# Performance work log

Measured on AMD Instinct MI355X. Metric: run time of the kernel, lower is better.

The kernel has to match this reference:

```python
import jax, jax.numpy as jnp
import numpy as np

N_HEADS = 8
N_POINTS = 4
EPS = 1e-5


def _conv1x1(x, w, b):
    # x: [B,C,H,W], w: [O,C]
    return jnp.einsum('bchw,oc->bohw', x, w) + b[None, :, None, None]


def _gn(x, g, b, groups=32):
    B, C, H, W = x.shape
    xr = x.reshape(B, groups, C // groups, H, W)
    m = xr.mean((2, 3, 4), keepdims=True)
    v = xr.var((2, 3, 4), keepdims=True)
    xn = ((xr - m) * jax.lax.rsqrt(v + EPS)).reshape(B, C, H, W)
    return xn * g[None, :, None, None] + b[None, :, None, None]


def _ln(x, g, b):
    m = x.mean(-1, keepdims=True)
    v = x.var(-1, keepdims=True)
    return (x - m) * jax.lax.rsqrt(v + EPS) * g + b


def _ln_spec(x, g2, b2, n):
    # modality-specific LayerNorm: separate params for v tokens [:n] and i tokens [n:]
    return jnp.concatenate([_ln(x[:, :n], g2[0], b2[0]), _ln(x[:, n:], g2[1], b2[1])], 1)


def _sine_pos(h, w, d):
    nf = d // 2
    scale = 2.0 * np.pi
    ye = jnp.arange(1, h + 1, dtype=jnp.float32) / h * scale
    xe = jnp.arange(1, w + 1, dtype=jnp.float32) / w * scale
    dim_t = 10000.0 ** (2.0 * (jnp.arange(nf) // 2).astype(jnp.float32) / nf)
    def enc(e):
        p = e[:, None] / dim_t
        return jnp.stack([jnp.sin(p[:, 0::2]), jnp.cos(p[:, 1::2])], -1).reshape(e.shape[0], nf)
    py = enc(ye)  # [h,nf]
    px = enc(xe)  # [w,nf]
    pos = jnp.concatenate([jnp.broadcast_to(py[:, None, :], (h, w, nf)),
                           jnp.broadcast_to(px[None, :, :], (h, w, nf))], -1)
    return pos.reshape(h * w, d)


def _bilinear(vl, loc):
    # vl: [B,h,w,Hd,Dh] value for one level, loc: [B,Lq,Hd,P,2] normalized (x,y)
    B, h, w, Hd, Dh = vl.shape
    Lq, P = loc.shape[1], loc.shape[3]
    x = loc[..., 0] * w - 0.5
    y = loc[..., 1] * h - 0.5
    x0 = jnp.floor(x)
    y0 = jnp.floor(y)
    wx = x - x0
    wy = y - y0
    x0i = x0.astype(jnp.int32)
    y0i = y0.astype(jnp.int32)
    v2 = vl.reshape(B, h * w, Hd, Dh).transpose(0, 2, 1, 3)  # [B,Hd,HW,Dh]
    def g(ix, iy):
        valid = ((ix >= 0) & (ix < w) & (iy >= 0) & (iy < h)).astype(vl.dtype)
        flat = jnp.clip(iy, 0, h - 1) * w + jnp.clip(ix, 0, w - 1)  # [B,Lq,Hd,P]
        idx = flat.transpose(0, 2, 1, 3).reshape(B, Hd, Lq * P)
        gv = jnp.take_along_axis(v2, idx[..., None], axis=2)  # [B,Hd,Lq*P,Dh]
        gv = gv.reshape(B, Hd, Lq, P, Dh).transpose(0, 2, 1, 3, 4)  # [B,Lq,Hd,P,Dh]
        return gv * valid[..., None]
    return (g(x0i, y0i) * ((1 - wx) * (1 - wy))[..., None]
            + g(x0i + 1, y0i) * (wx * (1 - wy))[..., None]
            + g(x0i, y0i + 1) * ((1 - wx) * wy)[..., None]
            + g(x0i + 1, y0i + 1) * (wx * wy)[..., None])


def _deform_attn(q, src, ref, shapes, ow, ob, aww, awb, vw, vb, opw, opb):
    B, Len, D = src.shape
    L = len(shapes)
    Hd, P = N_HEADS, N_POINTS
    Dh = D // Hd
    value = src @ vw + vb
    off = (q @ ow + ob).reshape(B, Len, Hd, L, P, 2)
    aw = jax.nn.softmax((q @ aww + awb).reshape(B, Len, Hd, L * P), -1).reshape(B, Len, Hd, L, P)
    norm = jnp.array([[s[1], s[0]] for s in shapes], jnp.float32)  # (w,h) per level
    loc = ref[None, :, None, None, None, :] + off / norm[None, None, None, :, None, :]
    out = jnp.zeros((B, Len, Hd, Dh), value.dtype)
    start = 0
    for l, (hh, ww) in enumerate(shapes):
        vl = value[:, start:start + hh * ww].reshape(B, hh, ww, Hd, Dh)
        samp = _bilinear(vl, loc[:, :, :, l])  # [B,Len,Hd,P,Dh]
        out = out + (samp * aw[:, :, :, l, :, None]).sum(3)
        start += hh * ww
    return out.reshape(B, Len, D) @ opw + opb


def _forward(input_v, input_i, av_w, av_b, av_g, av_be, ai_w, ai_b, ai_g, ai_be,
             level_embed, off_w, off_b, aw_w, aw_b, vp_w, vp_b, op_w, op_b,
             ln1_g, ln1_b, ffn1_w, ffn1_b, ffn2_w, ffn2_b, ln2_g, ln2_b,
             as_w, as_b, as_g, as_be):
    b, c, h, w = input_v.shape
    D = av_w.shape[0]
    hw = h * w
    fv = _gn(_conv1x1(input_v, av_w, av_b), av_g, av_be)
    fi = _gn(_conv1x1(input_i, ai_w, ai_b), ai_g, ai_be)
    sv = fv.reshape(b, D, hw).transpose(0, 2, 1)
    si = fi.reshape(b, D, hw).transpose(0, 2, 1)
    src = jnp.concatenate([sv, si], 1)  # [b, 2hw, D]
    pos = _sine_pos(h, w, D)
    posf = jnp.concatenate([pos + level_embed[0], pos + level_embed[1]], 0)
    gx = (jnp.arange(w, dtype=jnp.float32) + 0.5) / w
    gy = (jnp.arange(h, dtype=jnp.float32) + 0.5) / h
    X, Y = jnp.meshgrid(gx, gy)
    ref1 = jnp.stack([X, Y], -1).reshape(hw, 2)
    ref = jnp.concatenate([ref1, ref1], 0)  # [2hw, 2]
    shapes = [(h, w), (h, w)]
    for i in range(off_w.shape[0]):
        q = src + posf
        attn = _deform_attn(q, src, ref, shapes, off_w[i], off_b[i], aw_w[i], aw_b[i],
                            vp_w[i], vp_b[i], op_w[i], op_b[i])
        src = _ln_spec(src + attn, ln1_g[i], ln1_b[i], hw)
        ff = jax.nn.relu(src @ ffn1_w[i] + ffn1_b[i]) @ ffn2_w[i] + ffn2_b[i]
        src = _ln_spec(src + ff, ln2_g[i], ln2_b[i], hw)
    out = src[:, :hw] + src[:, hw:]  # chunk along tokens, sum modalities
    out = out.transpose(0, 2, 1).reshape(b, D, h, w)
    return _gn(_conv1x1(out, as_w, as_b), as_g, as_be)


def setup_inputs():
    key = jax.random.key(0)
    B, C, H, W = 16, 768, 20, 20
    D, NL, Hd, L, P, Dff = 512, 6, N_HEADS, 2, N_POINTS, 1024
    ks = iter(jax.random.split(key, 64))
    def rn(shape, scale=0.02):
        return jax.random.normal(next(ks), shape, jnp.float32) * scale
    return {
        'input_v': jax.random.normal(next(ks), (B, C, H, W), jnp.float32),
        'input_i': jax.random.normal(next(ks), (B, C, H, W), jnp.float32),
        'av_w': rn((D, C)), 'av_b': jnp.zeros((D,)), 'av_g': jnp.ones((D,)), 'av_be': jnp.zeros((D,)),
        'ai_w': rn((D, C)), 'ai_b': jnp.zeros((D,)), 'ai_g': jnp.ones((D,)), 'ai_be': jnp.zeros((D,)),
        'level_embed': rn((L, D)),
        'off_w': rn((NL, D, Hd * L * P * 2)), 'off_b': rn((NL, Hd * L * P * 2), 0.5),
        'aw_w': rn((NL, D, Hd * L * P)), 'aw_b': jnp.zeros((NL, Hd * L * P)),
        'vp_w': rn((NL, D, D)), 'vp_b': jnp.zeros((NL, D)),
        'op_w': rn((NL, D, D)), 'op_b': jnp.zeros((NL, D)),
        'ln1_g': jnp.ones((NL, 2, D)), 'ln1_b': jnp.zeros((NL, 2, D)),
        'ffn1_w': rn((NL, D, Dff)), 'ffn1_b': jnp.zeros((NL, Dff)),
        'ffn2_w': rn((NL, Dff, D)), 'ffn2_b': jnp.zeros((NL, D)),
        'ln2_g': jnp.ones((NL, 2, D)), 'ln2_b': jnp.zeros((NL, 2, D)),
        'as_w': rn((C, D)), 'as_b': jnp.zeros((C,)), 'as_g': jnp.ones((C,)), 'as_be': jnp.zeros((C,)),
    }


def reference(input_v, input_i, av_w, av_b, av_g, av_be, ai_w, ai_b, ai_g, ai_be,
              level_embed, off_w, off_b, aw_w, aw_b, vp_w, vp_b, op_w, op_b,
              ln1_g, ln1_b, ffn1_w, ffn1_b, ffn2_w, ffn2_b, ln2_g, ln2_b,
              as_w, as_b, as_g, as_be):
    return _forward(input_v, input_i, av_w, av_b, av_g, av_be, ai_w, ai_b, ai_g, ai_be,
                    level_embed, off_w, off_b, aw_w, aw_b, vp_w, vp_b, op_w, op_b,
                    ln1_g, ln1_b, ffn1_w, ffn1_b, ffn2_w, ffn2_b, ln2_g, ln2_b,
                    as_w, as_b, as_g, as_be)
```

## Files before the change

kernel.cpp:

```cpp
#include <hip/hip_runtime.h>
#include <hip/hip_bf16.h>
#include <cstddef>
#include <math.h>


constexpr int kB   = 16;
constexpr int kCin = 768;
constexpr int kHW  = 400;
constexpr int kWpx = 20;
constexpr int kHpx = 20;
constexpr int kD   = 512;
constexpr int kLen = 800;
constexpr int kDff = 1024;
constexpr int kNL  = 6;
constexpr float kEps = 1e-5f;

typedef __attribute__((ext_vector_type(8))) short s8v;
typedef __attribute__((ext_vector_type(4))) short s4v;
typedef __attribute__((ext_vector_type(4))) float f4v;

__device__ __forceinline__ int swzk(int row, int k) {
  return (k & ~31) | ((((k >> 3) + (row >> 1)) & 3) << 3) | (k & 7);
}

__device__ __forceinline__ unsigned short f2b(float f) {
  union { __hip_bfloat16 h; unsigned short u; } cv;
  cv.h = __float2bfloat16(f);
  return cv.u;
}

__device__ __forceinline__ float b2f(unsigned short u) {
  return __uint_as_float(((unsigned)u) << 16);
}

__device__ __forceinline__ void gll(const unsigned short* g, unsigned short* l) {
  __builtin_amdgcn_global_load_lds(
      (const __attribute__((address_space(1))) unsigned int*)g,
      (__attribute__((address_space(3))) unsigned int*)l, 16, 0, 0);
}

__device__ __forceinline__ void breduce2(float& s, float& s2, float* sh) {
#pragma unroll
  for (int o = 32; o > 0; o >>= 1) {
    s  += __shfl_down(s, o);
    s2 += __shfl_down(s2, o);
  }
  const int wid = threadIdx.x >> 6, lane = threadIdx.x & 63;
  if (lane == 0) { sh[wid] = s; sh[4 + wid] = s2; }
  __syncthreads();
  if (threadIdx.x == 0) {
    sh[0] = sh[0] + sh[1] + sh[2] + sh[3];
    sh[4] = sh[4] + sh[5] + sh[6] + sh[7];
  }
  __syncthreads();
  s = sh[0]; s2 = sh[4];
}

template<int EPI>
__global__ __launch_bounds__(256)
void mgemm(const unsigned short* __restrict__ Abf,
           const unsigned short* __restrict__ Bw,
           const float* __restrict__ bias,
           const unsigned short* __restrict__ resb,
           float* __restrict__ Cf, unsigned short* __restrict__ Cb2,
           const float* __restrict__ aux,
           unsigned short* __restrict__ Cb,
           int K, int ldc, int Nreal)
{
  __shared__ unsigned short As[3][4096];
  __shared__ unsigned short Bs[3][4096];
  const int tid = threadIdx.x;
  const int w = tid >> 6, l = tid & 63;

  const int gx = gridDim.x;
  const int nwg = gx * gridDim.y;
  const int bid = blockIdx.y * gx + blockIdx.x;
  const int q = nwg >> 3, r = nwg & 7;
  const int xcd = bid & 7, idx = bid >> 3;
  const int wgid = (xcd < r ? xcd * (q + 1) : r * (q + 1) + (xcd - r) * q) + idx;
  const int m0 = (wgid / gx) * 128;
  const int n0 = (wgid % gx) * 128;

  if (EPI == 6 && m0 >= 6400) { Bw = resb; bias = aux; }

  f4v acc[4][4] = {};

  const int srow = w * 32 + (l >> 2);
  const unsigned short* ga0 = Abf + (size_t)(m0 + srow) * K + (l & 3) * 8;
  const unsigned short* ga1 = ga0 + (size_t)16 * K;
  const unsigned short* gb0 = Bw + (size_t)(n0 + srow) * K + (l & 3) * 8;
  const unsigned short* gb1 = gb0 + (size_t)16 * K;
  const int lb0 = (w * 32) * 32;
  const int lb1 = (w * 32 + 16) * 32;

  int aoff[4], boff[4];
#pragma unroll
  for (int f = 0; f < 4; f++) {
    const int ra = (w >> 1) * 64 + f * 16 + (l & 15);
    aoff[f] = ra * 32 + ((((l >> 4) + (ra >> 1)) & 3) << 3);
    const int rb = (w & 1) * 64 + f * 16 + (l & 15);
    boff[f] = rb * 32 + ((((l >> 4) + (rb >> 1)) & 3) << 3);
  }

#define STAGEG(ko, bi) do { \
    gll(ga0 + (ko), &As[bi][lb0]); gll(ga1 + (ko), &As[bi][lb1]); \
    gll(gb0 + (ko), &Bs[bi][lb0]); gll(gb1 + (ko), &Bs[bi][lb1]); } while (0)

  const int NT = K >> 5;
  STAGEG(0, 0);
  STAGEG(32, 1);

  int cur = 0;
  int bpre = 2;
  int kpre = 64;
  for (int t = 0; t < NT; ++t) {
    if (t + 1 < NT) asm volatile("s_waitcnt vmcnt(4)" ::: "memory");
    else            asm volatile("s_waitcnt vmcnt(0)" ::: "memory");
    __builtin_amdgcn_s_barrier();
    __builtin_amdgcn_sched_barrier(0);
    if (t + 2 < NT) STAGEG(kpre, bpre);
    s8v af[4], bf4[4];
#pragma unroll
    for (int f = 0; f < 4; f++) {
      af[f]  = *(const s8v*)&As[cur][aoff[f]];
      bf4[f] = *(const s8v*)&Bs[cur][boff[f]];
    }
    __builtin_amdgcn_s_setprio(1);
#pragma unroll
    for (int i = 0; i < 4; i++)
#pragma unroll
      for (int j = 0; j < 4; j++)
        acc[i][j] = __builtin_amdgcn_mfma_f32_16x16x32_bf16(af[i], bf4[j], acc[i][j], 0, 0, 0);
    __builtin_amdgcn_s_setprio(0);
    kpre += 32;
    bpre = (bpre == 2) ? 0 : bpre + 1;
    cur  = (cur == 2) ? 0 : cur + 1;
  }
#undef STAGEG

  const int colb = n0 + (w & 1) * 64;
  const int rowb = m0 + (w >> 1) * 64 + (l >> 4) * 4;
#pragma unroll
  for (int i = 0; i < 4; i++) {
#pragma unroll
    for (int j = 0; j < 4; j++) {
      const int col = colb + j * 16 + (l & 15);
      float bv;
      if (EPI == 4) bv = (col < kD) ? bias[col] : 0.0f;
      else          bv = bias[col];
#pragma unroll
      for (int r2 = 0; r2 < 4; r2++) {
        const int row = rowb + i * 16 + r2;
        float v = acc[i][j][r2] + bv;
        if (EPI == 1) {
          Cb[(size_t)row * ldc + swzk(row, col)] = f2b(fmaxf(v, 0.0f));
        } else if (EPI == 2) {
          v += b2f(resb[(size_t)row * kD + swzk(row, col)]);
          Cb[(size_t)row * kD + col] = f2b(v);
        } else if (EPI == 3) {
          const int bb = row / kHW, p = row % kHW;
          Cb[((size_t)bb * Nreal + col) * kHW + p] = f2b(v);
        } else if (EPI == 4) {
          if (col < kD) {
            Cb[(size_t)row * kD + col] = f2b(v);
          } else {
            const int c = col - kD;
            if (c < 192)
              Cb2[(size_t)row * 192 + c] = f2b(v + aux[(size_t)(row % kLen) * 192 + c]);
          }
        } else if (EPI == 5) {
          if (row < kLen) {
            const int ll = col >> 8, c = col & 255;
            if (c < 192)
              Cf[(((size_t)ll * kLen) + row) * 192 + c] = v;
          }
        } else {
          Cb[(size_t)row * kD + col] = f2b(v);
        }
      }
    }
  }
}

__device__ __forceinline__ void cvt8t(const float* __restrict__ W,
                                      unsigned short* __restrict__ out,
                                      int K, int N, int g)
{
  const int n = g % N;
  const int k = (g / N) * 8;
  s8v p;
#pragma unroll
  for (int j = 0; j < 8; j++) p[j] = (short)f2b(W[(size_t)(k + j) * N + n]);
  const int base = n * K + (k & ~31) + ((((k >> 3) + (n >> 1)) & 3) << 3);
  *(s8v*)&out[base] = p;
}

__global__ __launch_bounds__(256)
void cvt_all_k(const float* __restrict__ vp_w, const float* __restrict__ op_w,
               const float* __restrict__ off_w, const float* __restrict__ aw_w,
               const float* __restrict__ f1w_a, const float* __restrict__ f2w_a,
               unsigned short* __restrict__ wall)
{
  const int lyr = blockIdx.x / 832;
  int g = (blockIdx.x % 832) * 256 + threadIdx.x;
  unsigned short* wl = wall + (size_t)lyr * 1703936;
  if (g < 32768) { cvt8t(vp_w + (size_t)lyr * kD * kD, wl, 512, 512, g); return; }
  g -= 32768;
  if (g < 16384) {
    const int n = g & 255;
    const int k = (g >> 8) * 8;
    const float* ow  = off_w + (size_t)lyr * kD * 128;
    const float* aww = aw_w  + (size_t)lyr * kD * 64;
    s8v p;
#pragma unroll
    for (int j = 0; j < 8; j++) {
      float v = 0.0f;
      if (n < 128)      v = ow[(size_t)(k + j) * 128 + n];
      else if (n < 192) v = aww[(size_t)(k + j) * 64 + (n - 128)];
      p[j] = (short)f2b(v);
    }
    const int row = 512 + n;
    const int base = row * 512 + (k & ~31) + ((((k >> 3) + (row >> 1)) & 3) << 3);
    *(s8v*)&wl[base] = p;
    return;
  }
  g -= 16384;
  if (g < 32768) { cvt8t(op_w + (size_t)lyr * kD * kD, wl + 393216, 512, 512, g); return; }
  g -= 32768;
  if (g < 65536) { cvt8t(f1w_a + (size_t)lyr * kD * kDff, wl + 655360, 512, 1024, g); return; }
  g -= 65536;
  cvt8t(f2w_a + (size_t)lyr * kDff * kD, wl + 1179648, 1024, 512, g);
}

__global__ __launch_bounds__(256)
void pre_k(const float* __restrict__ level_embed,
           const float* __restrict__ off_w, const float* __restrict__ aw_w,
           const float* __restrict__ off_b, const float* __restrict__ aw_b,
           unsigned short* __restrict__ posfb,
           unsigned short* __restrict__ woaw_all, float* __restrict__ biasall)
{
  int g = blockIdx.x * 256 + threadIdx.x;
  if (g < 57344) {
    const int d0 = (g & 63) * 8;
    const int t  = g >> 6;
    s8v o;
    if (t >= kLen) {
#pragma unroll
      for (int j = 0; j < 8; j++) o[j] = 0;
    } else {
      const int lvl = t / kHW;
      const int tt = t % kHW;
      const int yy = tt / kWpx, xx = tt % kWpx;
#pragma unroll
      for (int j = 0; j < 8; j++) {
        const int d = d0 + j;
        const int dd = d & 255;
        const float e = (d < 256) ? ((float)(yy + 1) * (6.283185307179586f / kHpx))
                                  : ((float)(xx + 1) * (6.283185307179586f / kWpx));
        const float dimt = powf(10000.0f, (float)(dd >> 1) / 128.0f);
        const float pp = e / dimt;
        const float val = (dd & 1) ? cosf(pp) : sinf(pp);
        o[j] = (short)f2b(val + level_embed[lvl * kD + d]);
      }
    }
    *(s8v*)&posfb[(size_t)t * kD + swzk(t, d0)] = o;
    return;
  }
  g -= 57344;
  if (g < 98304) {
    const int l = g >> 14;
    const int gg = g & 16383;
    const int n = gg & 255;
    const int k = (gg >> 8) * 8;
    const float* ow = off_w + (size_t)l * kD * 128;
    const float* aww = aw_w + (size_t)l * kD * 64;
    s8v p;
#pragma unroll
    for (int j = 0; j < 8; j++) {
      float v = 0.0f;
      if (n < 128)      v = ow[(size_t)(k + j) * 128 + n];
      else if (n < 192) v = aww[(size_t)(k + j) * 64 + (n - 128)];
      p[j] = (short)f2b(v);
    }
    const int row = l * 256 + n;
    const int base = row * 512 + (k & ~31) + ((((k >> 3) + (row >> 1)) & 3) << 3);
    *(s8v*)&woaw_all[base] = p;
    return;
  }
  g -= 98304;
  if (g < 1536) {
    const int l = g >> 8, c = g & 255;
    float v = 0.0f;
    if (c < 128)      v = off_b[l * 128 + c];
    else if (c < 192) v = aw_b[l * 64 + (c - 128)];
    biasall[l * 256 + c] = v;
  }
}

__global__ void tincvt_k(const float* __restrict__ inv, const float* __restrict__ ini,
                         const float* __restrict__ W0, const float* __restrict__ W1,
                         unsigned short* __restrict__ out, unsigned short* __restrict__ wcs)
{
  __shared__ float t[16][17];
  const int bid = blockIdx.x;
  if (bid < 38400) {
    const int z = bid / 1200;
    const int rem = bid % 1200;
    const int c0 = (rem % 48) * 16, p0 = (rem / 48) * 16;
    const int mod = z >> 4, b = z & 15;
    const float* in = (mod ? ini : inv) + (size_t)b * kCin * kHW;
    const int tx = threadIdx.x & 15, ty = threadIdx.x >> 4;
    t[ty][tx] = in[((size_t)(c0 + ty)) * kHW + p0 + tx];
    __syncthreads();
    const int row = z * kHW + p0 + ty;
    const int c = c0 + tx;
    out[(size_t)row * kCin + swzk(row, c)] = f2b(t[tx][ty]);
    return;
  }
  int gid = (bid - 38400) * 256 + threadIdx.x;
  const float* W = W0;
  unsigned short* o = wcs;
  if (gid >= 49152) { gid -= 49152; W = W1; o = wcs + 393216; }
  const int n = gid / 96;
  const int k = (gid % 96) * 8;
  s8v p;
#pragma unroll
  for (int j = 0; j < 8; j++) p[j] = (short)f2b(W[(size_t)n * kCin + k + j]);
  const int base = n * kCin + (k & ~31) + ((((k >> 3) + (n >> 1)) & 3) << 3);
  *(s8v*)&o[base] = p;
}

__global__ __launch_bounds__(256)
void gn_stats_tok_k(const unsigned short* __restrict__ x, float* __restrict__ stats)
{
  __shared__ float sh[8];
  const int mb = blockIdx.x >> 5;
  const int g = blockIdx.x & 31;
  const unsigned short* xb = x + (size_t)mb * kHW * kD + g * 16;
  float s = 0.f, s2 = 0.f;
  for (int i = threadIdx.x; i < 800; i += 256) {
    const int p = i >> 1, half = i & 1;
    const s8v u = *(const s8v*)&xb[(size_t)p * kD + half * 8];
#pragma unroll
    for (int j = 0; j < 8; j++) {
      const float v = b2f((unsigned short)u[j]);
      s += v; s2 += v * v;
    }
  }
  breduce2(s, s2, sh);
  if (threadIdx.x == 0) {
    const float mean = s / (kHW * 16.0f);
    const float var  = s2 / (kHW * 16.0f) - mean * mean;
    stats[blockIdx.x * 2]     = mean;
    stats[blockIdx.x * 2 + 1] = rsqrtf(var + kEps);
  }
}

__global__ void gn_norm_tok_k(const unsigned short* __restrict__ x,
                              unsigned short* __restrict__ srcb,
                              const float* __restrict__ stats,
                              const float* __restrict__ gv, const float* __restrict__ bev,
                              const float* __restrict__ gi, const float* __restrict__ bei)
{
  const int gid = blockIdx.x * 256 + threadIdx.x;
  const int d0 = (gid & 63) * 8;
  const int rl = gid >> 6;
  const int mb = rl / kHW;
  const int p  = rl - mb * kHW;
  const int mod = mb >> 4, b = mb & 15;
  const int g = d0 >> 4;
  const float mean = stats[(mb * 32 + g) * 2];
  const float rstd = stats[(mb * 32 + g) * 2 + 1];
  const float* gam = mod ? gi : gv;
  const float* bet = mod ? bei : bev;
  const s8v u = *(const s8v*)&x[(size_t)rl * kD + d0];
  const int row = b * kLen + mod * kHW + p;
  s8v o;
#pragma unroll
  for (int j = 0; j < 8; j++)
    o[j] = (short)f2b((b2f((unsigned short)u[j]) - mean) * rstd * gam[d0 + j] + bet[d0 + j]);
  *(s8v*)&srcb[(size_t)row * kD + swzk(row, d0)] = o;
}

__global__ __launch_bounds__(256)
void gn_stats_ch_k(const unsigned short* __restrict__ x, float* __restrict__ stats)
{
  __shared__ float sh[8];
  const int b = blockIdx.x >> 5;
  const int g = blockIdx.x & 31;
  const unsigned short* xb = x + (size_t)b * kCin * kHW + (size_t)g * 24 * kHW;
  float s = 0.f, s2 = 0.f;
  for (int i = threadIdx.x; i < 1200; i += 256) {
    const s8v u = *(const s8v*)&xb[(size_t)i * 8];
#pragma unroll
    for (int j = 0; j < 8; j++) {
      const float v = b2f((unsigned short)u[j]);
      s += v; s2 += v * v;
    }
  }
  breduce2(s, s2, sh);
  if (threadIdx.x == 0) {
    const float mean = s / (24.0f * kHW);
    const float var  = s2 / (24.0f * kHW) - mean * mean;
    stats[blockIdx.x * 2]     = mean;
    stats[blockIdx.x * 2 + 1] = rsqrtf(var + kEps);
  }
}

__global__ void gn_norm_ch_k(const unsigned short* __restrict__ x, float* __restrict__ out,
                             const float* __restrict__ stats,
                             const float* __restrict__ gam, const float* __restrict__ bet)
{
  const int gid = blockIdx.x * 256 + threadIdx.x;
  const int idx8 = gid * 8;
  const int rest = idx8 / kHW;
  const int c = rest % kCin;
  const int b = rest / kCin;
  const int g = c / 24;
  const float mean = stats[(b * 32 + g) * 2];
  const float rstd = stats[(b * 32 + g) * 2 + 1];
  const float gg = gam[c], bb = bet[c];
  const s8v u = *(const s8v*)&x[idx8];
  float4 o0, o1;
  o0.x = (b2f((unsigned short)u[0]) - mean) * rstd * gg + bb;
  o0.y = (b2f((unsigned short)u[1]) - mean) * rstd * gg + bb;
  o0.z = (b2f((unsigned short)u[2]) - mean) * rstd * gg + bb;
  o0.w = (b2f((unsigned short)u[3]) - mean) * rstd * gg + bb;
  o1.x = (b2f((unsigned short)u[4]) - mean) * rstd * gg + bb;
  o1.y = (b2f((unsigned short)u[5]) - mean) * rstd * gg + bb;
  o1.z = (b2f((unsigned short)u[6]) - mean) * rstd * gg + bb;
  o1.w = (b2f((unsigned short)u[7]) - mean) * rstd * gg + bb;
  *(float4*)(out + idx8)     = o0;
  *(float4*)(out + idx8 + 4) = o1;
}

__global__ __launch_bounds__(256)
void ln4_k(const unsigned short* __restrict__ x, unsigned short* __restrict__ outb,
           const float* __restrict__ gamma, const float* __restrict__ beta)
{
  const int row = blockIdx.x * 4 + (threadIdx.x >> 6);
  const int l = threadIdx.x & 63;
  const int mod = ((row % kLen) < kHW) ? 0 : 1;
  const s8v u = *(const s8v*)&x[(size_t)row * kD + l * 8];
  float v[8];
#pragma unroll
  for (int j = 0; j < 8; j++) v[j] = b2f((unsigned short)u[j]);
  float s = 0.f, s2 = 0.f;
#pragma unroll
  for (int j = 0; j < 8; j++) { s += v[j]; s2 += v[j] * v[j]; }
#pragma unroll
  for (int o = 32; o > 0; o >>= 1) {
    s  += __shfl_xor(s, o);
    s2 += __shfl_xor(s2, o);
  }
  const float mean = s * (1.0f / kD);
  const float var  = s2 * (1.0f / kD) - mean * mean;
  const float rstd = rsqrtf(var + kEps);
  const float* g  = gamma + mod * kD + l * 8;
  const float* be = beta  + mod * kD + l * 8;
  s8v o8;
#pragma unroll
  for (int j = 0; j < 8; j++)
    o8[j] = (short)f2b((v[j] - mean) * rstd * g[j] + be[j]);
  *(s8v*)&outb[(size_t)row * kD + swzk(row, l * 8)] = o8;
}

__global__ __launch_bounds__(256)
void sample_k(const unsigned short* __restrict__ value,
              const unsigned short* __restrict__ offaw,
              unsigned short* __restrict__ out)
{
  __shared__ float wls[2][64][8];
  const int tid = threadIdx.x;
  const int tok = tid >> 7;
  const int wt  = tid & 127;
  const int token = blockIdx.x * 2 + tok;
  const int b = token / kLen;
  const int t = token % kLen;
  const int tt = t % kHW;

  if (wt < 64) {
    const int h = wt >> 3, lp = wt & 7, lvl = lp >> 2, p = lp & 3;
    const unsigned short* oa = offaw + (size_t)token * 192;
    const float lg = b2f(oa[128 + h * 8 + lp]);
    float mx = lg;
#pragma unroll
    for (int msk = 1; msk < 8; msk <<= 1) mx = fmaxf(mx, __shfl_xor(mx, msk));
    const float ex = __expf(lg - mx);
    float ssum = ex;
#pragma unroll
    for (int msk = 1; msk < 8; msk <<= 1) ssum += __shfl_xor(ssum, msk);
    const float aw = ex / ssum;

    const float x = (float)(tt % kWpx) + b2f(oa[h * 16 + lvl * 8 + p * 2]);
    const float y = (float)(tt / kWpx) + b2f(oa[h * 16 + lvl * 8 + p * 2 + 1]);
    const float x0f = floorf(x), y0f = floorf(y);
    const float wx = x - x0f, wy = y - y0f;
    const int x0 = (int)x0f, y0 = (int)y0f;
    const int rowbase = b * kLen + lvl * kHW;
#pragma unroll
    for (int dy = 0; dy < 2; dy++) {
#pragma unroll
      for (int dx = 0; dx < 2; dx++) {
        const int ix = x0 + dx, iy = y0 + dy;
        const bool valid = (ix >= 0) & (ix < kWpx) & (iy >= 0) & (iy < kHpx);
        const float cw = (dx ? wx : 1.0f - wx) * (dy ? wy : 1.0f - wy);
        const float w = valid ? aw * cw : 0.0f;
        const int ixc = min(max(ix, 0), kWpx - 1);
        const int iyc = min(max(iy, 0), kHpx - 1);
        const int r = rowbase + iyc * kWpx + ixc;
        const int cn = dy * 2 + dx;
        wls[tok][wt][cn * 2]     = w;
        wls[tok][wt][cn * 2 + 1] = __int_as_float(r);
      }
    }
  }
  __syncthreads();

  const int c0 = wt * 4;
  const int h = wt >> 4;
  float acc0 = 0.f, acc1 = 0.f, acc2 = 0.f, acc3 = 0.f;
  const unsigned short* vb = value + c0;
#pragma unroll
  for (int pp = 0; pp < 8; pp++) {
    const float* wl = wls[tok][h * 8 + pp];
#pragma unroll
    for (int cn = 0; cn < 4; cn++) {
      const float w = wl[cn * 2];
      const int r = __float_as_int(wl[cn * 2 + 1]);
      const s4v q = *(const s4v*)(vb + (size_t)r * kD);
      acc0 += w * b2f((unsigned short)q[0]);
      acc1 += w * b2f((unsigned short)q[1]);
      acc2 += w * b2f((unsigned short)q[2]);
      acc3 += w * b2f((unsigned short)q[3]);
    }
  }
  const int sk = swzk(token, c0);
  s4v o;
  o[0] = (short)f2b(acc0); o[1] = (short)f2b(acc1);
  o[2] = (short)f2b(acc2); o[3] = (short)f2b(acc3);
  *(s4v*)&out[(size_t)token * kD + sk] = o;
}

__global__ void sumcvt_k(const unsigned short* __restrict__ srcb,
                         unsigned short* __restrict__ tokb,
                         const float* __restrict__ asw,
                         unsigned short* __restrict__ wcs)
{
  const int bid = blockIdx.x;
  if (bid < 1600) {
    const int gid = bid * 256 + threadIdx.x;
    const int d0 = (gid & 63) * 8;
    const int rest = gid >> 6;
    const int b = rest / kHW, p = rest % kHW;
    const int r1 = b * kLen + p;
    const int r2 = r1 + kHW;
    const int ro = b * kHW + p;
    const s8v u1 = *(const s8v*)&srcb[(size_t)r1 * kD + swzk(r1, d0)];
    const s8v u2 = *(const s8v*)&srcb[(size_t)r2 * kD + swzk(r2, d0)];
    s8v o;
#pragma unroll
    for (int j = 0; j < 8; j++)
      o[j] = (short)f2b(b2f((unsigned short)u1[j]) + b2f((unsigned short)u2[j]));
    *(s8v*)&tokb[(size_t)ro * kD + swzk(ro, d0)] = o;
    return;
  }
  const int gid = (bid - 1600) * 256 + threadIdx.x;
  const int n = gid / 64;
  const int k = (gid % 64) * 8;
  s8v p;
#pragma unroll
  for (int j = 0; j < 8; j++) p[j] = (short)f2b(asw[(size_t)n * kD + k + j]);
  const int base = n * kD + (k & ~31) + ((((k >> 3) + (n >> 1)) & 3) << 3);
  *(s8v*)&wcs[base] = p;
}

extern "C" void kernel_launch(void* const* d_in, const int* in_sizes, int n_in,
                              void* d_out, int out_size, void* d_ws, size_t ws_size,
                              hipStream_t stream)
{
  const float* input_v     = (const float*)d_in[0];
  const float* input_i     = (const float*)d_in[1];
  const float* av_w        = (const float*)d_in[2];
  const float* av_b        = (const float*)d_in[3];
  const float* av_g        = (const float*)d_in[4];
  const float* av_be       = (const float*)d_in[5];
  const float* ai_w        = (const float*)d_in[6];
  const float* ai_b        = (const float*)d_in[7];
  const float* ai_g        = (const float*)d_in[8];
  const float* ai_be       = (const float*)d_in[9];
  const float* level_embed = (const float*)d_in[10];
  const float* off_w       = (const float*)d_in[11];
  const float* off_b       = (const float*)d_in[12];
  const float* aw_w        = (const float*)d_in[13];
  const float* aw_b        = (const float*)d_in[14];
  const float* vp_w        = (const float*)d_in[15];
  const float* vp_b        = (const float*)d_in[16];
  const float* op_w        = (const float*)d_in[17];
  const float* op_b        = (const float*)d_in[18];
  const float* ln1_g       = (const float*)d_in[19];
  const float* ln1_b       = (const float*)d_in[20];
  const float* ffn1_w      = (const float*)d_in[21];
  const float* ffn1_b      = (const float*)d_in[22];
  const float* ffn2_w      = (const float*)d_in[23];
  const float* ffn2_b      = (const float*)d_in[24];
  const float* ln2_g       = (const float*)d_in[25];
  const float* ln2_b       = (const float*)d_in[26];
  const float* as_w        = (const float*)d_in[27];
  const float* as_b        = (const float*)d_in[28];
  const float* as_g        = (const float*)d_in[29];
  const float* as_be       = (const float*)d_in[30];

  unsigned short* offawb = (unsigned short*)d_ws;
  float* posWc   = (float*)(offawb + 2457600);
  float* biasall = posWc   + (size_t)921600;
  float* stats   = biasall + (size_t)1536;
  unsigned short* srcb     = (unsigned short*)(stats + 2048);
  unsigned short* bufA     = srcb     + (size_t)6553600;
  unsigned short* bufB     = bufA     + (size_t)13107200;
  unsigned short* wall     = bufB     + (size_t)6553600;
  unsigned short* wcs      = wall     + (size_t)10223616;
  unsigned short* woaw_all = wcs      + (size_t)786432;
  unsigned short* posfb    = woaw_all + (size_t)786432;
  unsigned short* wallb = wall;

  const int M = kB * kLen;

  pre_k<<<dim3(614), 256, 0, stream>>>(level_embed, off_w, aw_w, off_b, aw_b,
                                       posfb, woaw_all, biasall);
  mgemm<5><<<dim3(12, 7), 256, 0, stream>>>(
      posfb, woaw_all, biasall, nullptr, posWc, nullptr, nullptr, nullptr,
      512, 0, 0);

  tincvt_k<<<dim3(38784), 256, 0, stream>>>(input_v, input_i, av_w, ai_w,
                                            bufA, wcs);
  mgemm<6><<<dim3(4, 100), 256, 0, stream>>>(
      bufA, wcs, av_b, wcs + 393216, nullptr, nullptr, ai_b, bufB, 768, 512, 0);
  gn_stats_tok_k<<<dim3(1024), 256, 0, stream>>>(bufB, stats);
  gn_norm_tok_k<<<dim3(3200), 256, 0, stream>>>(
      bufB, srcb, stats, av_g, av_be, ai_g, ai_be);

  cvt_all_k<<<dim3(4992), 256, 0, stream>>>(vp_w, op_w, off_w, aw_w,
                                            ffn1_w, ffn2_w, wall);

  for (int l = 0; l < kNL; l++) {
    unsigned short* wcomb = wall + (size_t)l * 1703936;
    unsigned short* wop   = wcomb + 393216;
    unsigned short* wf1   = wcomb + 655360;
    unsigned short* wf2   = wcomb + 1179648;
    const float* vbl  = vp_b   + (size_t)l * kD;
    const float* opbl = op_b   + (size_t)l * kD;
    const float* l1g  = ln1_g  + (size_t)l * 2 * kD;
    const float* l1b  = ln1_b  + (size_t)l * 2 * kD;
    const float* f1b  = ffn1_b + (size_t)l * kDff;
    const float* f2b_ = ffn2_b + (size_t)l * kD;
    const float* l2g  = ln2_g  + (size_t)l * 2 * kD;
    const float* l2b  = ln2_b  + (size_t)l * 2 * kD;

    mgemm<4><<<dim3(6, 100), 256, 0, stream>>>(
        srcb, wcomb, vbl, nullptr, nullptr, offawb, posWc + (size_t)l * 153600,
        bufA, 512, 0, 0);

    sample_k<<<dim3(M / 2), 256, 0, stream>>>(bufA, offawb, bufB);

    mgemm<2><<<dim3(4, 100), 256, 0, stream>>>(
        bufB, wop, opbl, srcb, nullptr, nullptr, nullptr, bufA, 512, 512, 0);

    ln4_k<<<dim3(M / 4), 256, 0, stream>>>(bufA, srcb, l1g, l1b);

    mgemm<1><<<dim3(8, 100), 256, 0, stream>>>(
        srcb, wf1, f1b, nullptr, nullptr, nullptr, nullptr, bufA, 512, 1024, 0);
    mgemm<2><<<dim3(4, 100), 256, 0, stream>>>(
        bufA, wf2, f2b_, srcb, nullptr, nullptr, nullptr, bufB, 1024, 512, 0);

    ln4_k<<<dim3(M / 4), 256, 0, stream>>>(bufB, srcb, l2g, l2b);
  }

  sumcvt_k<<<dim3(1792), 256, 0, stream>>>(srcb, bufA, as_w, wcs);
  mgemm<3><<<dim3(6, 50), 256, 0, stream>>>(
      bufA, wcs, as_b, nullptr, nullptr, nullptr, nullptr, wallb, 512, 0, 768);
  gn_stats_ch_k<<<dim3(kB * 32), 256, 0, stream>>>(wallb, stats);
  gn_norm_ch_k<<<dim3(2400), 256, 0, stream>>>(
      wallb, (float*)d_out, stats, as_g, as_be);
}
```

Before: 1.069 ms.

## Restructure GEMM to two waves with 64x128 per-wave tiles and wave-specialized loading

The 128x128 GEMM tile is now computed by two waves instead of four. Each wave owns a 64x128 output sub-tile with 32 accumulators, so every B fragment read from LDS feeds more MFMAs. Global-to-LDS staging is split so wave 0 loads A and wave 1 loads B, eight chunks each, and the vmcnt wait is adjusted to match. The trade is fewer waves per block to hide latency, much higher register pressure from the doubled accumulator count, and launch bounds changed to 128 threads with two blocks per CU.

Result: slower. 1.202 ms (+12.4%).

```diff
diff --git a/kernel.cpp b/kernel.cpp
--- a/kernel.cpp
+++ b/kernel.cpp
@@ -57,7 +57,7 @@
 }
 
 template<int EPI>
-__global__ __launch_bounds__(256)
+__global__ __launch_bounds__(128, 2)
 void mgemm(const unsigned short* __restrict__ Abf,
            const unsigned short* __restrict__ Bw,
            const float* __restrict__ bias,
@@ -67,8 +67,7 @@
            unsigned short* __restrict__ Cb,
            int K, int ldc, int Nreal)
 {
-  __shared__ unsigned short As[3][4096];
-  __shared__ unsigned short Bs[3][4096];
+  __shared__ unsigned short LDS[3][8192];
   const int tid = threadIdx.x;
   const int w = tid >> 6, l = tid & 63;
 
@@ -83,68 +82,67 @@
 
   if (EPI == 6 && m0 >= 6400) { Bw = resb; bias = aux; }
 
-  f4v acc[4][4] = {};
-
-  const int srow = w * 32 + (l >> 2);
-  const unsigned short* ga0 = Abf + (size_t)(m0 + srow) * K + (l & 3) * 8;
-  const unsigned short* ga1 = ga0 + (size_t)16 * K;
-  const unsigned short* gb0 = Bw + (size_t)(n0 + srow) * K + (l & 3) * 8;
-  const unsigned short* gb1 = gb0 + (size_t)16 * K;
-  const int lb0 = (w * 32) * 32;
-  const int lb1 = (w * 32 + 16) * 32;
-
-  int aoff[4], boff[4];
-#pragma unroll
-  for (int f = 0; f < 4; f++) {
-    const int ra = (w >> 1) * 64 + f * 16 + (l & 15);
-    aoff[f] = ra * 32 + ((((l >> 4) + (ra >> 1)) & 3) << 3);
-    const int rb = (w & 1) * 64 + f * 16 + (l & 15);
-    boff[f] = rb * 32 + ((((l >> 4) + (rb >> 1)) & 3) << 3);
-  }
-
-#define STAGEG(ko, bi) do { \
-    gll(ga0 + (ko), &As[bi][lb0]); gll(ga1 + (ko), &As[bi][lb1]); \
-    gll(gb0 + (ko), &Bs[bi][lb0]); gll(gb1 + (ko), &Bs[bi][lb1]); } while (0)
+  f4v acc[4][8] = {};
+
+  const unsigned short* gsrc =
+      (w == 0 ? Abf + (size_t)(m0 + (l >> 2)) * K
+              : Bw  + (size_t)(n0 + (l >> 2)) * K) + (l & 3) * 8;
+  const int wsel = w ? 4096 : 0;
+
+  auto STAGE = [&](int ko, int bi) {
+#pragma unroll
+    for (int c = 0; c < 8; c++)
+      gll(gsrc + (size_t)(c * 16) * K + ko, &LDS[bi][wsel + c * 512]);
+  };
+
+  int aoff[4], boff[8];
+#pragma unroll
+  for (int i = 0; i < 4; i++) {
+    const int ra = w * 64 + i * 16 + (l & 15);
+    aoff[i] = ra * 32 + ((((l >> 4) + (ra >> 1)) & 3) << 3);
+  }
+#pragma unroll
+  for (int j = 0; j < 8; j++) {
+    const int rb = j * 16 + (l & 15);
+    boff[j] = 4096 + rb * 32 + ((((l >> 4) + (rb >> 1)) & 3) << 3);
+  }
 
   const int NT = K >> 5;
-  STAGEG(0, 0);
-  STAGEG(32, 1);
+  STAGE(0, 0);
+  STAGE(32, 1);
 
   int cur = 0;
   int bpre = 2;
   int kpre = 64;
   for (int t = 0; t < NT; ++t) {
-    if (t + 1 < NT) asm volatile("s_waitcnt vmcnt(4)" ::: "memory");
+    if (t + 1 < NT) asm volatile("s_waitcnt vmcnt(8)" ::: "memory");
     else            asm volatile("s_waitcnt vmcnt(0)" ::: "memory");
     __builtin_amdgcn_s_barrier();
     __builtin_amdgcn_sched_barrier(0);
-    if (t + 2 < NT) STAGEG(kpre, bpre);
-    s8v af[4], bf4[4];
-#pragma unroll
-    for (int f = 0; f < 4; f++) {
-      af[f]  = *(const s8v*)&As[cur][aoff[f]];
-      bf4[f] = *(const s8v*)&Bs[cur][boff[f]];
-    }
+    if (t + 2 < NT) STAGE(kpre, bpre);
+    s8v af[4], bf8[8];
+#pragma unroll
+    for (int i = 0; i < 4; i++) af[i] = *(const s8v*)&LDS[cur][aoff[i]];
+#pragma unroll
+    for (int j = 0; j < 8; j++) bf8[j] = *(const s8v*)&LDS[cur][boff[j]];
     __builtin_amdgcn_s_setprio(1);
 #pragma unroll
     for (int i = 0; i < 4; i++)
 #pragma unroll
-      for (int j = 0; j < 4; j++)
-        acc[i][j] = __builtin_amdgcn_mfma_f32_16x16x32_bf16(af[i], bf4[j], acc[i][j], 0, 0, 0);
+      for (int j = 0; j < 8; j++)
+        acc[i][j] = __builtin_amdgcn_mfma_f32_16x16x32_bf16(af[i], bf8[j], acc[i][j], 0, 0, 0);
     __builtin_amdgcn_s_setprio(0);
     kpre += 32;
     bpre = (bpre == 2) ? 0 : bpre + 1;
     cur  = (cur == 2) ? 0 : cur + 1;
   }
-#undef STAGEG
-
-  const int colb = n0 + (w & 1) * 64;
-  const int rowb = m0 + (w >> 1) * 64 + (l >> 4) * 4;
+
+  const int rowb = m0 + w * 64 + (l >> 4) * 4;
 #pragma unroll
   for (int i = 0; i < 4; i++) {
 #pragma unroll
-    for (int j = 0; j < 4; j++) {
-      const int col = colb + j * 16 + (l & 15);
+    for (int j = 0; j < 8; j++) {
+      const int col = n0 + j * 16 + (l & 15);
       float bv;
       if (EPI == 4) bv = (col < kD) ? bias[col] : 0.0f;
       else          bv = bias[col];
@@ -628,13 +626,13 @@
 
   pre_k<<<dim3(614), 256, 0, stream>>>(level_embed, off_w, aw_w, off_b, aw_b,
                                        posfb, woaw_all, biasall);
-  mgemm<5><<<dim3(12, 7), 256, 0, stream>>>(
+  mgemm<5><<<dim3(12, 7), 128, 0, stream>>>(
       posfb, woaw_all, biasall, nullptr, posWc, nullptr, nullptr, nullptr,
       512, 0, 0);
 
   tincvt_k<<<dim3(38784), 256, 0, stream>>>(input_v, input_i, av_w, ai_w,
                                             bufA, wcs);
-  mgemm<6><<<dim3(4, 100), 256, 0, stream>>>(
+  mgemm<6><<<dim3(4, 100), 128, 0, stream>>>(
       bufA, wcs, av_b, wcs + 393216, nullptr, nullptr, ai_b, bufB, 768, 512, 0);
   gn_stats_tok_k<<<dim3(1024), 256, 0, stream>>>(bufB, stats);
   gn_norm_tok_k<<<dim3(3200), 256, 0, stream>>>(
@@ -657,27 +655,27 @@
     const float* l2g  = ln2_g  + (size_t)l * 2 * kD;
     const float* l2b  = ln2_b  + (size_t)l * 2 * kD;
 
-    mgemm<4><<<dim3(6, 100), 256, 0, stream>>>(
+    mgemm<4><<<dim3(6, 100), 128, 0, stream>>>(
         srcb, wcomb, vbl, nullptr, nullptr, offawb, posWc + (size_t)l * 153600,
         bufA, 512, 0, 0);
 
     sample_k<<<dim3(M / 2), 256, 0, stream>>>(bufA, offawb, bufB);
 
-    mgemm<2><<<dim3(4, 100), 256, 0, stream>>>(
+    mgemm<2><<<dim3(4, 100), 128, 0, stream>>>(
         bufB, wop, opbl, srcb, nullptr, nullptr, nullptr, bufA, 512, 512, 0);
 
     ln4_k<<<dim3(M / 4), 256, 0, stream>>>(bufA, srcb, l1g, l1b);
 
-    mgemm<1><<<dim3(8, 100), 256, 0, stream>>>(
+    mgemm<1><<<dim3(8, 100), 128, 0, stream>>>(
         srcb, wf1, f1b, nullptr, nullptr, nullptr, nullptr, bufA, 512, 1024, 0);
-    mgemm<2><<<dim3(4, 100), 256, 0, stream>>>(
+    mgemm<2><<<dim3(4, 100), 128, 0, stream>>>(
         bufA, wf2, f2b_, srcb, nullptr, nullptr, nullptr, bufB, 1024, 512, 0);
 
     ln4_k<<<dim3(M / 4), 256, 0, stream>>>(bufB, srcb, l2g, l2b);
   }
 
   sumcvt_k<<<dim3(1792), 256, 0, stream>>>(srcb, bufA, as_w, wcs);
-  mgemm<3><<<dim3(6, 50), 256, 0, stream>>>(
+  mgemm<3><<<dim3(6, 50), 128, 0, stream>>>(
       bufA, wcs, as_b, nullptr, nullptr, nullptr, nullptr, wallb, 512, 0, 768);
   gn_stats_ch_k<<<dim3(kB * 32), 256, 0, stream>>>(wallb, stats);
   gn_norm_ch_k<<<dim3(2400), 256, 0, stream>>>(
```
